# Kernel tuning notes

Hardware: AMD Instinct MI355X
Metric: run time of the kernel (lower is better)

## Reference

```python
import math
import jax, jax.numpy as jnp
import numpy as np

B, C_IN, C_OUT, K, STYLE, H, W = 16, 512, 512, 3, 512, 64, 64


def setup_inputs() -> dict:
    key = jax.random.key(0)
    k1, k2, k3, k4 = jax.random.split(key, 4)
    return {
        "x": jax.random.normal(k1, (B, C_IN, H, W), jnp.float32),
        "style": jax.random.normal(k2, (B, STYLE), jnp.float32),
        "weight": jax.random.normal(k3, (C_OUT, C_IN, K, K), jnp.float32),  # learned conv weight (leading 1 dim of torch param squeezed)
        "mod_w": jax.random.normal(k4, (C_IN, STYLE), jnp.float32),         # EqualLinear weight
        "mod_b": jnp.ones((C_IN,), jnp.float32),                             # EqualLinear bias (bias_init=1)
    }


def reference(x, style, weight, mod_w, mod_b):
    # EqualLinear modulation: scale = 1/sqrt(style_dim), lr_mul = 1
    mod_scale = 1.0 / math.sqrt(STYLE)
    s = style @ (mod_w.T * mod_scale) + mod_b            # [B, C_IN]

    # per-sample modulated weight
    w_scale = 1.0 / math.sqrt(C_IN * K * K)
    w = w_scale * weight[None] * s[:, None, :, None, None]  # [B, C_OUT, C_IN, K, K]

    # demodulate
    demod = jax.lax.rsqrt(jnp.sum(w * w, axis=(2, 3, 4)) + 1e-8)  # [B, C_OUT]
    w = w * demod[:, :, None, None, None]

    pad = K // 2

    def conv_one(xi, wi):
        # xi: [C_IN, H, W], wi: [C_OUT, C_IN, K, K]
        return jax.lax.conv_general_dilated(
            xi[None], wi, window_strides=(1, 1),
            padding=[(pad, pad), (pad, pad)],
            dimension_numbers=("NCHW", "OIHW", "NCHW"),
        )[0]

    return jax.vmap(conv_one)(x, w)  # [B, C_OUT, H, W]
```

## Files before the change

### kernel.cpp

```cpp
#include <hip/hip_runtime.h>
#include <hip/hip_bf16.h>
#include <math.h>
#include <stdint.h>

#define B_     16
#define CI_    512
#define CO_    512
#define HH     64
#define WW     64
#define STYLE_ 512

typedef __bf16 bf16x8 __attribute__((ext_vector_type(8)));
typedef float f32x16 __attribute__((ext_vector_type(16)));

__device__ __forceinline__ int fsl(int r, int h) {
    return (2 * r + (h ^ ((r >> 2) & 1))) ^ (((r >> 4) & 1) << 1);
}

#define WS_S     0
#define WS_DEMOD 32768
#define WS_WSQ   65536
#define WS_WB    1114112
#define WS_XS    5832704

__device__ __forceinline__ void gload16(const void* g, void* l) {
    __builtin_amdgcn_global_load_lds((const __attribute__((address_space(1))) uint32_t*)g,
                                     (__attribute__((address_space(3))) uint32_t*)l, 16, 0, 0);
}

__global__ __launch_bounds__(256) void k_style2(const float* __restrict__ style,
                                                const float* __restrict__ mod_w,
                                                const float* __restrict__ mod_b,
                                                float* __restrict__ s_out) {
    const int ci   = blockIdx.x * 4 + (threadIdx.x >> 6);
    const int b    = blockIdx.y;
    const int lane = threadIdx.x & 63;
    const float4* mw = (const float4*)(mod_w + (size_t)ci * STYLE_);
    const float4* st = (const float4*)(style + (size_t)b * STYLE_);
    float acc = 0.f;
    #pragma unroll
    for (int i = 0; i < 2; ++i) {
        float4 a = mw[lane + i * 64], s = st[lane + i * 64];
        acc += a.x * s.x + a.y * s.y + a.z * s.z + a.w * s.w;
    }
    #pragma unroll
    for (int off = 32; off >= 1; off >>= 1) acc += __shfl_xor(acc, off);
    if (lane == 0)
        s_out[b * CI_ + ci] = acc * 0.044194173824159216f + mod_b[ci];
}

__global__ __launch_bounds__(256) void k_wprep(const float* __restrict__ weight,
                                               float* __restrict__ wsq, __bf16* __restrict__ wb) {
    int p = blockIdx.x * 256 + threadIdx.x;
    int co = p >> 9, ci = p & 511;
    const float* wp = weight + (size_t)p * 9;
    const int gs = ((co >> 6) << 7) + fsl(co & 63, (ci >> 3) & 1);
    float acc = 0.f;
    #pragma unroll
    for (int t = 0; t < 9; ++t) {
        float v = wp[t];
        acc += v * v;
        wb[(((size_t)(ci >> 4) * 9 + t) * 8192) + gs * 8 + (ci & 7)] = (__bf16)v;
    }
    wsq[(size_t)ci * CO_ + co] = acc;
}

__global__ void k_demod(const float* __restrict__ s, const float* __restrict__ wsq,
                        float* __restrict__ demod) {
    int b = blockIdx.x, co = threadIdx.x;
    const float w_scale2 = 1.0f / 4608.0f;
    float acc = 0.f;
    const float* sb = s + b * CI_;
    for (int ci = 0; ci < CI_; ++ci) { float sv = sb[ci]; acc += sv * sv * wsq[(size_t)ci * CO_ + co]; }
    demod[b * CO_ + co] = 1.0f / sqrtf(acc * w_scale2 + 1e-8f);
}

__global__ __launch_bounds__(256) void k_xs(const float* __restrict__ x, const float* __restrict__ s,
                                            __bf16* __restrict__ xs) {
    __shared__ float Lt[64][65];
    const int y = blockIdx.x, b = blockIdx.y;
    const int tid = threadIdx.x;
    const float w_scale = 0.014731391274719739f;
    for (int ci0 = 0; ci0 < CI_; ci0 += 64) {
        for (int i = tid; i < 64 * 16; i += 256) {
            int ci = i >> 4, x4 = (i & 15) * 4;
            const float4 v = *(const float4*)&x[((size_t)(b * CI_ + ci0 + ci) * HH + y) * WW + x4];
            float sc = s[b * CI_ + ci0 + ci] * w_scale;
            Lt[ci][x4]     = v.x * sc;
            Lt[ci][x4 + 1] = v.y * sc;
            Lt[ci][x4 + 2] = v.z * sc;
            Lt[ci][x4 + 3] = v.w * sc;
        }
        __syncthreads();
        for (int o = tid; o < 512; o += 256) {
            int xx = o >> 3, oct = o & 7;
            int cb = ci0 + oct * 8;
            int chunk = cb >> 4;
            int pp = fsl(xx + 1, oct & 1) - 2;
            bf16x8 v;
            #pragma unroll
            for (int j = 0; j < 8; ++j) v[j] = (__bf16)Lt[oct * 8 + j][xx];
            size_t idx = (((size_t)chunk * 16 + b) * 66 + (y + 1)) * 1024 + pp * 8;
            *(bf16x8*)&xs[idx] = v;
        }
        __syncthreads();
    }
    if (y == 0 || y == 63) {
        const int row = (y == 0) ? 0 : 65;
        uint32_t* xs32 = (uint32_t*)xs;
        for (int c = 0; c < 32; ++c)
            for (int i = tid; i < 512; i += 256)
                xs32[(((size_t)c * 16 + b) * 66 + row) * 512 + i] = 0;
    }
}

#define XBUF 21120
#define WBUF 18432

__global__ __launch_bounds__(256, 2) void k_conv(
    const __bf16* __restrict__ xs, const __bf16* __restrict__ wb,
    const float* __restrict__ demod, float* __restrict__ out)
{
    __shared__ __align__(128) char smem[2 * XBUF + 2 * WBUF];

    const int tid  = threadIdx.x;
    const int lane = tid & 63;
    const int wave = tid >> 6;

    const int bid  = blockIdx.x;
    const int r8   = bid & 7;
    const int q    = bid >> 3;
    const int co0  = (q & 7) * 64;
    const int tt   = q >> 3;
    const int y0   = (tt & 7) * 8;
    const int b    = r8 * 2 + (tt >> 3);

    const int lm = lane & 31;
    const int g2 = lane >> 5;

    for (int i = tid; i < 320; i += 256) {
        int buf = i / 160, rem = i % 160;
        int rb = rem >> 4, hh = rem & 15;
        int side = hh >> 3, dw = hh & 7;
        ((uint32_t*)smem)[buf * (XBUF / 4) + rb * 528 + side * 520 + dw] = 0;
    }
    asm volatile("s_waitcnt lgkmcnt(0)" ::: "memory");

    uint32_t soff[10];
    uint32_t sdst[10];
    if (wave < 2) {
        #pragma unroll
        for (int i = 0; i < 10; ++i) {
            int j = wave * 10 + i, rb = j >> 1, seg = j & 1;
            soff[i] = (uint32_t)((y0 + rb) * 1024 + seg * 512 + lane * 8);
            sdst[i] = (uint32_t)(rb * 2112 + 32 + seg * 1024 + lane * 16);
        }
    } else {
        #pragma unroll
        for (int i = 0; i < 9; ++i) {
            int j = (wave - 2) * 9 + i;
            int tap = j >> 1, seg = j & 1;
            soff[i] = (uint32_t)(tap * 8192 + co0 * 16 + seg * 512 + lane * 8);
            sdst[i] = (uint32_t)(j * 1024 + lane * 16);
        }
        soff[9] = 0; sdst[9] = 0;
    }

    const uint32_t acol = (uint32_t)(16 * fsl(lm, g2));
    uint32_t cbase[3];
    #pragma unroll
    for (int kw = 0; kw < 3; ++kw) cbase[kw] = (uint32_t)(16 * fsl(lm + kw, g2));
    uint32_t rbase[4];
    #pragma unroll
    for (int rr = 0; rr < 4; ++rr) rbase[rr] = (uint32_t)((2 * wave + rr) * 2112);

    f32x16 acc[2][4];
    #pragma unroll
    for (int mi = 0; mi < 2; ++mi)
        #pragma unroll
        for (int n = 0; n < 4; ++n)
            #pragma unroll
            for (int r = 0; r < 16; ++r) acc[mi][n][r] = 0.f;

    auto stage = [&](int chunk, int sel) {
        if (wave < 2) {
            const __bf16* base = xs + (size_t)chunk * 1081344 + (size_t)b * 67584;
            #pragma unroll
            for (int i = 0; i < 10; ++i) gload16(base + soff[i], smem + sel * XBUF + sdst[i]);
        } else {
            const __bf16* base = wb + (size_t)chunk * 73728;
            #pragma unroll
            for (int i = 0; i < 9; ++i) gload16(base + soff[i], smem + 2 * XBUF + sel * WBUF + sdst[i]);
        }
    };

    stage(0, 0);

    for (int t = 0; t < 32; ++t) {
        if (t < 31) {
            stage(t + 1, (t + 1) & 1);
            if (wave < 2) asm volatile("s_waitcnt vmcnt(10)" ::: "memory");
            else          asm volatile("s_waitcnt vmcnt(9)"  ::: "memory");
        } else {
            asm volatile("s_waitcnt vmcnt(0)" ::: "memory");
        }
        __builtin_amdgcn_s_barrier();

        const char* xbuf = smem + (t & 1) * XBUF;
        const char* wbuf = smem + 2 * XBUF + (t & 1) * WBUF + acol;

        __builtin_amdgcn_s_setprio(1);
        #pragma unroll
        for (int kw = 0; kw < 3; ++kw) {
            bf16x8 fa[3][2], fb[4][2];
            #pragma unroll
            for (int kh = 0; kh < 3; ++kh) {
                const char* wp = wbuf + (kh * 3 + kw) * 2048;
                fa[kh][0] = *(const bf16x8*)(wp);
                fa[kh][1] = *(const bf16x8*)(wp + 1024);
            }
            #pragma unroll
            for (int rr = 0; rr < 4; ++rr) {
                fb[rr][0] = *(const bf16x8*)(xbuf + rbase[rr] + cbase[kw]);
                fb[rr][1] = *(const bf16x8*)(xbuf + rbase[rr] + cbase[kw] + 1024);
            }
            #pragma unroll
            for (int kh = 0; kh < 3; ++kh)
                #pragma unroll
                for (int ys = 0; ys < 2; ++ys)
                    #pragma unroll
                    for (int nt = 0; nt < 2; ++nt) {
                        acc[0][ys * 2 + nt] = __builtin_amdgcn_mfma_f32_32x32x16_bf16(
                            fa[kh][0], fb[ys + kh][nt], acc[0][ys * 2 + nt], 0, 0, 0);
                        acc[1][ys * 2 + nt] = __builtin_amdgcn_mfma_f32_32x32x16_bf16(
                            fa[kh][1], fb[ys + kh][nt], acc[1][ys * 2 + nt], 0, 0, 0);
                    }
        }
        __builtin_amdgcn_s_setprio(0);
        __builtin_amdgcn_s_barrier();
    }

    #pragma unroll
    for (int mi = 0; mi < 2; ++mi) {
        #pragma unroll
        for (int ys = 0; ys < 2; ++ys) {
            const int y = y0 + 2 * wave + ys;
            float* outb = out + ((size_t)b * CO_ + co0 + mi * 32) * 4096 + (size_t)y * 64;
            #pragma unroll
            for (int reg = 0; reg < 16; ++reg) {
                const int cosub = (reg & 3) + 8 * (reg >> 2) + 4 * g2;
                const float dm = demod[b * CO_ + co0 + mi * 32 + cosub];
                outb[(size_t)cosub * 4096 + lm]      = acc[mi][ys * 2 + 0][reg] * dm;
                outb[(size_t)cosub * 4096 + 32 + lm] = acc[mi][ys * 2 + 1][reg] * dm;
            }
        }
    }
}

extern "C" void kernel_launch(void* const* d_in, const int* in_sizes, int n_in,
                              void* d_out, int out_size, void* d_ws, size_t ws_size,
                              hipStream_t stream) {
    const float* x      = (const float*)d_in[0];
    const float* style  = (const float*)d_in[1];
    const float* weight = (const float*)d_in[2];
    const float* mod_w  = (const float*)d_in[3];
    const float* mod_b  = (const float*)d_in[4];
    float* out = (float*)d_out;

    char* wsb = (char*)d_ws;
    float*  s_buf = (float*)(wsb + WS_S);
    float*  demod = (float*)(wsb + WS_DEMOD);
    float*  wsq   = (float*)(wsb + WS_WSQ);
    __bf16* wb    = (__bf16*)(wsb + WS_WB);
    __bf16* xs    = (__bf16*)(wsb + WS_XS);

    k_style2<<<dim3(CI_ / 4, B_), dim3(256), 0, stream>>>(style, mod_w, mod_b, s_buf);
    k_wprep<<<dim3(CO_ * CI_ / 256), dim3(256), 0, stream>>>(weight, wsq, wb);
    k_demod<<<dim3(B_), dim3(CO_), 0, stream>>>(s_buf, wsq, demod);
    k_xs<<<dim3(HH, B_), dim3(256), 0, stream>>>(x, s_buf, xs);
    k_conv<<<dim3(1024), dim3(256), 0, stream>>>(xs, wb, demod, out);
}
```

Baseline: 319.7 us.

## Split K-chunk loop into three barrier-separated phases interleaving loads and MFMA

Restructures the main loop into three per-kw phases. Each phase issues LDS fragment loads, then a barrier and lgkmcnt wait, then runs its MFMA block at raised priority. The next chunk's global-to-LDS staging is issued inside the first phase, and the vmcnt wait moves to the end of the third phase, so global loads get a full chunk of compute to hide behind. The goal is finer-grained overlap and synchronized waves, at the cost of more barriers per iteration (six instead of two).

```diff
diff --git a/kernel.cpp b/kernel.cpp
--- a/kernel.cpp
+++ b/kernel.cpp
@@ -144,7 +144,6 @@
         int side = hh >> 3, dw = hh & 7;
         ((uint32_t*)smem)[buf * (XBUF / 4) + rb * 528 + side * 520 + dw] = 0;
     }
-    asm volatile("s_waitcnt lgkmcnt(0)" ::: "memory");
 
     uint32_t soff[10];
     uint32_t sdst[10];
@@ -195,50 +194,59 @@
     };
 
     stage(0, 0);
+    asm volatile("s_waitcnt vmcnt(0) lgkmcnt(0)" ::: "memory");
+    __builtin_amdgcn_s_barrier();
+
+#define PHASE(KW, STAGE_STMT, TAIL_STMT)                                          \
+    {                                                                             \
+        bf16x8 fa[3][2], fb[4][2];                                                \
+        _Pragma("unroll")                                                         \
+        for (int kh = 0; kh < 3; ++kh) {                                          \
+            const char* wp = wbuf + (kh * 3 + (KW)) * 2048;                       \
+            fa[kh][0] = *(const bf16x8*)(wp);                                     \
+            fa[kh][1] = *(const bf16x8*)(wp + 1024);                              \
+        }                                                                         \
+        _Pragma("unroll")                                                         \
+        for (int rr = 0; rr < 4; ++rr) {                                          \
+            fb[rr][0] = *(const bf16x8*)(xbuf + rbase[rr] + cbase[KW]);           \
+            fb[rr][1] = *(const bf16x8*)(xbuf + rbase[rr] + cbase[KW] + 1024);    \
+        }                                                                         \
+        STAGE_STMT;                                                               \
+        __builtin_amdgcn_s_barrier();                                             \
+        asm volatile("s_waitcnt lgkmcnt(0)" ::: "memory");                        \
+        __builtin_amdgcn_sched_barrier(0);                                        \
+        __builtin_amdgcn_s_setprio(1);                                            \
+        _Pragma("unroll")                                                         \
+        for (int kh = 0; kh < 3; ++kh)                                            \
+            _Pragma("unroll")                                                     \
+            for (int ys = 0; ys < 2; ++ys)                                        \
+                _Pragma("unroll")                                                 \
+                for (int nt = 0; nt < 2; ++nt) {                                  \
+                    acc[0][ys * 2 + nt] = __builtin_amdgcn_mfma_f32_32x32x16_bf16(\
+                        fa[kh][0], fb[ys + kh][nt], acc[0][ys * 2 + nt], 0, 0, 0);\
+                    acc[1][ys * 2 + nt] = __builtin_amdgcn_mfma_f32_32x32x16_bf16(\
+                        fa[kh][1], fb[ys + kh][nt], acc[1][ys * 2 + nt], 0, 0, 0);\
+                }                                                                 \
+        __builtin_amdgcn_s_setprio(0);                                            \
+        TAIL_STMT;                                                                \
+        __builtin_amdgcn_s_barrier();                                             \
+    }
 
     for (int t = 0; t < 32; ++t) {
-        if (t < 31) {
-            stage(t + 1, (t + 1) & 1);
-            if (wave < 2) asm volatile("s_waitcnt vmcnt(10)" ::: "memory");
-            else          asm volatile("s_waitcnt vmcnt(9)"  ::: "memory");
-        } else {
-            asm volatile("s_waitcnt vmcnt(0)" ::: "memory");
-        }
-        __builtin_amdgcn_s_barrier();
-
         const char* xbuf = smem + (t & 1) * XBUF;
         const char* wbuf = smem + 2 * XBUF + (t & 1) * WBUF + acol;
 
-        __builtin_amdgcn_s_setprio(1);
-        #pragma unroll
-        for (int kw = 0; kw < 3; ++kw) {
-            bf16x8 fa[3][2], fb[4][2];
-            #pragma unroll
-            for (int kh = 0; kh < 3; ++kh) {
-                const char* wp = wbuf + (kh * 3 + kw) * 2048;
-                fa[kh][0] = *(const bf16x8*)(wp);
-                fa[kh][1] = *(const bf16x8*)(wp + 1024);
-            }
-            #pragma unroll
-            for (int rr = 0; rr < 4; ++rr) {
-                fb[rr][0] = *(const bf16x8*)(xbuf + rbase[rr] + cbase[kw]);
-                fb[rr][1] = *(const bf16x8*)(xbuf + rbase[rr] + cbase[kw] + 1024);
-            }
-            #pragma unroll
-            for (int kh = 0; kh < 3; ++kh)
-                #pragma unroll
-                for (int ys = 0; ys < 2; ++ys)
-                    #pragma unroll
-                    for (int nt = 0; nt < 2; ++nt) {
-                        acc[0][ys * 2 + nt] = __builtin_amdgcn_mfma_f32_32x32x16_bf16(
-                            fa[kh][0], fb[ys + kh][nt], acc[0][ys * 2 + nt], 0, 0, 0);
-                        acc[1][ys * 2 + nt] = __builtin_amdgcn_mfma_f32_32x32x16_bf16(
-                            fa[kh][1], fb[ys + kh][nt], acc[1][ys * 2 + nt], 0, 0, 0);
-                    }
-        }
-        __builtin_amdgcn_s_setprio(0);
-        __builtin_amdgcn_s_barrier();
-    }
+        if (t < 31) {
+            PHASE(0, stage(t + 1, (t + 1) & 1), );
+            PHASE(1, , );
+            PHASE(2, , asm volatile("s_waitcnt vmcnt(0)" ::: "memory"));
+        } else {
+            PHASE(0, , );
+            PHASE(1, , );
+            PHASE(2, , );
+        }
+    }
+#undef PHASE
 
     #pragma unroll
     for (int mi = 0; mi < 2; ++mi) {
```

New measurement: 320.6 us. No clear change (+0.3%).
